# Optimization experiments

Measured on AMD Instinct MI355X. Metric: run time of the kernel, lower is better.

The kernel has to match this reference:

```python
import jax, jax.numpy as jnp
import numpy as np

N_NODES = 200000
N_EDGES = 6400000
N_GRAPHS = 512
VOCAB = 10
EMBED = 8
RLEN = 20
EPS = 1e-5


def setup_inputs() -> dict:
    key = jax.random.key(0)
    ks = jax.random.split(key, 16)
    f = lambda i, shape, s: jax.random.normal(ks[i], shape, jnp.float32) * s
    return {
        "x": jax.random.normal(ks[0], (N_NODES, 3), jnp.float32),
        "W1": f(1, (3, 64), 0.5), "b1": jnp.zeros((64,), jnp.float32),
        "gamma1": jnp.ones((64,), jnp.float32), "beta1": jnp.zeros((64,), jnp.float32),
        "W2": f(2, (64, 64), 0.12), "b2": jnp.zeros((64,), jnp.float32),
        "gamma2": jnp.ones((64,), jnp.float32), "beta2": jnp.zeros((64,), jnp.float32),
        "emb": f(3, (VOCAB, EMBED), 1.0),
        "conv_w": f(4, (16, EMBED, 3), 0.2), "conv_b": jnp.zeros((16,), jnp.float32),
        "fc_w": f(5, (16 * RLEN, 64), 0.06), "fc_b": jnp.zeros((64,), jnp.float32),
        "m1_w": f(6, (192, 128), 0.08), "m1_b": jnp.zeros((128,), jnp.float32),
        "m2_w": f(7, (128, 64), 0.1), "m2_b": jnp.zeros((64,), jnp.float32),
        "m3_w": f(8, (64, 3), 0.17), "m3_b": jnp.zeros((3,), jnp.float32),
        "edge_index": jax.random.randint(ks[9], (2, N_EDGES), 0, N_NODES),
        "batch": jnp.sort(jax.random.randint(ks[10], (N_NODES,), 0, N_GRAPHS)),
        "recipe": jax.random.randint(ks[11], (N_GRAPHS, RLEN), 0, VOCAB),
    }


def _gcn_aggregate(h, src, dst, dinv, n):
    # symmetric-normalized scatter-add: sum_j (d_i d_j)^{-1/2} h_j
    norm = dinv[src] * dinv[dst]
    return jax.ops.segment_sum(h[src] * norm[:, None], dst, num_segments=n)


def _bn(h, gamma, beta):
    mu = h.mean(0)
    var = h.var(0)  # biased variance, as torch BN uses for normalization
    return (h - mu) * jax.lax.rsqrt(var + EPS) * gamma + beta


def reference(x, W1, b1, gamma1, beta1, W2, b2, gamma2, beta2, emb,
              conv_w, conv_b, fc_w, fc_b, m1_w, m1_b, m2_w, m2_b, m3_w, m3_b,
              edge_index, batch, recipe):
    n = x.shape[0]
    loop = jnp.arange(n)
    src = jnp.concatenate([edge_index[0], loop])  # add self loops (GCNConv default)
    dst = jnp.concatenate([edge_index[1], loop])
    deg = jax.ops.segment_sum(jnp.ones_like(src, jnp.float32), dst, num_segments=n)
    dinv = jnp.where(deg > 0, jax.lax.rsqrt(deg), 0.0)

    h = _gcn_aggregate(x @ W1, src, dst, dinv, n) + b1
    h = jax.nn.relu(_bn(h, gamma1, beta1))
    h = _gcn_aggregate(h @ W2, src, dst, dinv, n) + b2
    h = jax.nn.relu(_bn(h, gamma2, beta2))

    counts = jax.ops.segment_sum(jnp.ones((n,), jnp.float32), batch, num_segments=N_GRAPHS)
    h_mean = jax.ops.segment_sum(h, batch, num_segments=N_GRAPHS) / jnp.maximum(counts, 1.0)[:, None]
    h_max = jax.ops.segment_max(h, batch, num_segments=N_GRAPHS)
    h_max = jnp.where(jnp.isfinite(h_max), h_max, 0.0)  # guard empty graphs
    h_graph = jnp.concatenate([h_mean, h_max], axis=1)  # [G, 128]

    r = emb[recipe].transpose(0, 2, 1)  # [G, embed, L]
    rc = jax.lax.conv_general_dilated(r, conv_w, window_strides=(1,), padding=[(1, 1)],
                                      dimension_numbers=("NCH", "OIH", "NCH"))
    rc = jax.nn.relu(rc + conv_b[None, :, None])  # [G, 16, L]
    r_flat = rc.reshape(rc.shape[0], -1)  # channel-major flatten, matches torch
    r_vec = jax.nn.relu(r_flat @ fc_w + fc_b)  # [G, 64]

    c = jnp.concatenate([h_graph, r_vec], axis=1)  # [G, 192]
    c = jax.nn.relu(c @ m1_w + m1_b)
    c = jax.nn.relu(c @ m2_w + m2_b)
    return c @ m3_w + m3_b  # [G, 3]
```

## Files before the change

kernel.cpp:

```cpp
#include <hip/hip_runtime.h>

#define N_NODES 200000
#define N_EDGES 6400000
#define N_GRAPHS 512
#define RLEN 20
#define EMBED 8
#define EPS 1e-5f

#define NPB 1024
#define NBKT ((N_NODES + NPB - 1) / NPB)
#define CHUNK 4096
#define CAP 36864

typedef unsigned short ushort_t;
typedef __attribute__((ext_vector_type(8))) short short8;
typedef __attribute__((ext_vector_type(4))) float f32x4;

__device__ inline ushort_t f32_to_bf16(float f) {
  unsigned u = __float_as_uint(f);
  unsigned r = (u + 0x7fff + ((u >> 16) & 1)) >> 16;
  return (ushort_t)r;
}
__device__ inline float bf16_to_f32(ushort_t us) {
  return __uint_as_float(((unsigned)us) << 16);
}
__device__ inline float bfu_lo(unsigned u) { return __uint_as_float(u << 16); }
__device__ inline float bfu_hi(unsigned u) { return __uint_as_float(u & 0xFFFF0000u); }


__global__ void k_binit(int* __restrict__ bcursor) {
  int b = threadIdx.x;
  if (b < NBKT) bcursor[b] = b * CAP;
}

__global__ void __launch_bounds__(256) k_bscatter(const int* __restrict__ src,
                                                  const int* __restrict__ dst,
                                                  int* __restrict__ bcursor,
                                                  int* __restrict__ ebuf) {
  __shared__ int hist[256];
  __shared__ int scanb[256];
  __shared__ int gbase[NBKT];
  __shared__ int staged[CHUNK];
  __shared__ int addrs[CHUNK];
  __shared__ int s_total;
  int t = threadIdx.x;
  int e0 = blockIdx.x * CHUNK;
  hist[t] = 0;
  __syncthreads();

  int pk[16], bk[16], rk[16];
  #pragma unroll
  for (int k = 0; k < 16; ++k) {
    int idx = e0 + t + k * 256;
    bk[k] = -1;
    if (idx < N_EDGES) {
      int s = src[idx], d = dst[idx];
      int b = d >> 10;
      pk[k] = s | ((d & (NPB - 1)) << 18);
      bk[k] = b;
      rk[k] = atomicAdd(&hist[b], 1);
    }
  }
  __syncthreads();
  int hv = hist[t];
  scanb[t] = hv;
  __syncthreads();
  for (int off = 1; off < 256; off <<= 1) {
    int u = (t >= off) ? scanb[t - off] : 0;
    __syncthreads();
    scanb[t] += u;
    __syncthreads();
  }
  int offt = scanb[t] - hv;
  if (t < NBKT && hv > 0) gbase[t] = atomicAdd(&bcursor[t], hv);
  if (t == 255) s_total = scanb[255];
  __syncthreads();
  hist[t] = offt;
  __syncthreads();
  #pragma unroll
  for (int k = 0; k < 16; ++k) {
    if (bk[k] >= 0) {
      int slot = hist[bk[k]] + rk[k];
      staged[slot] = pk[k];
      addrs[slot] = gbase[bk[k]] + rk[k];
    }
  }
  __syncthreads();
  int total = s_total;
  for (int i = t; i < total; i += 256)
    ebuf[addrs[i]] = staged[i];
}

__global__ void __launch_bounds__(256) k_bfill(const int* __restrict__ bcursor,
                                               const int* __restrict__ ebuf,
                                               const float* __restrict__ x,
                                               int* __restrict__ rowstart,
                                               int* __restrict__ rowlen,
                                               float* __restrict__ dinv,
                                               float4* __restrict__ xs,
                                               int* __restrict__ cols) {
  __shared__ int deg[NPB];
  __shared__ int cur[NPB];
  __shared__ int wsum[4];
  int b = blockIdx.x;
  int t = threadIdx.x;
  int lane = t & 63, wid = t >> 6;
  int estart = b * CAP;
  int eend = bcursor[b];
  for (int i = t; i < NPB; i += 256) deg[i] = 0;
  __syncthreads();
  for (int i = estart + t; i < eend; i += 256) {
    int p = ebuf[i];
    atomicAdd(&deg[((unsigned)p) >> 18], 1);
  }
  __syncthreads();
  int d0 = deg[t * 4], d1 = deg[t * 4 + 1], d2 = deg[t * 4 + 2], d3 = deg[t * 4 + 3];
  int tsum = d0 + d1 + d2 + d3;
  int incl = tsum;
  #pragma unroll
  for (int off = 1; off < 64; off <<= 1) {
    int u = __shfl_up(incl, off);
    if (lane >= off) incl += u;
  }
  if (lane == 63) wsum[wid] = incl;
  int wexcl = incl - tsum;
  __syncthreads();
  int wbase = 0;
  for (int w = 0; w < wid; ++w) wbase += wsum[w];
  int ebase = wbase + wexcl;
  cur[t * 4 + 0] = ebase;
  cur[t * 4 + 1] = ebase + d0;
  cur[t * 4 + 2] = ebase + d0 + d1;
  cur[t * 4 + 3] = ebase + d0 + d1 + d2;
  __syncthreads();
  #pragma unroll
  for (int k = 0; k < 4; ++k) {
    int dl = t * 4 + k;
    int n = b * NPB + dl;
    if (n < N_NODES) {
      rowstart[n] = estart + cur[dl];
      rowlen[n] = deg[dl];
      float dv = rsqrtf((float)(deg[dl] + 1));
      dinv[n] = dv;
      float4 v;
      v.x = x[n * 3 + 0] * dv;
      v.y = x[n * 3 + 1] * dv;
      v.z = x[n * 3 + 2] * dv;
      v.w = 0.f;
      xs[n] = v;
    }
  }
  __syncthreads();
  for (int i = estart + t; i < eend; i += 256) {
    int p = ebuf[i];
    int dl = ((unsigned)p) >> 18;
    int lpos = atomicAdd(&cur[dl], 1);
    cols[estart + lpos] = p & 0x3FFFF;
  }
}


__global__ void k_agg1(const float4* __restrict__ xs, float4* __restrict__ t,
                       const int* __restrict__ rowstart, const int* __restrict__ rowlen,
                       const int* __restrict__ cols,
                       const float* __restrict__ dinv, float* __restrict__ mom) {
  int n = blockIdx.x * blockDim.x + threadIdx.x;
  float m9[9] = {0.f, 0.f, 0.f, 0.f, 0.f, 0.f, 0.f, 0.f, 0.f};
  if (n < N_NODES) {
    float4 self = xs[n];
    float a0 = self.x, a1 = self.y, a2 = self.z;
    float b0 = 0.f, b1 = 0.f, b2 = 0.f;
    float c0 = 0.f, c1 = 0.f, c2 = 0.f;
    float e0 = 0.f, e1 = 0.f, e2 = 0.f;
    int base = rowstart[n];
    int len = rowlen[n];
    int j = 0;
    for (; j + 8 <= len; j += 8) {
      int s0 = cols[base + j],     s1 = cols[base + j + 1];
      int s2 = cols[base + j + 2], s3 = cols[base + j + 3];
      int s4 = cols[base + j + 4], s5 = cols[base + j + 5];
      int s6 = cols[base + j + 6], s7 = cols[base + j + 7];
      float4 v0 = xs[s0], v1 = xs[s1], v2 = xs[s2], v3 = xs[s3];
      float4 v4 = xs[s4], v5 = xs[s5], v6 = xs[s6], v7 = xs[s7];
      a0 += v0.x + v4.x; a1 += v0.y + v4.y; a2 += v0.z + v4.z;
      b0 += v1.x + v5.x; b1 += v1.y + v5.y; b2 += v1.z + v5.z;
      c0 += v2.x + v6.x; c1 += v2.y + v6.y; c2 += v2.z + v6.z;
      e0 += v3.x + v7.x; e1 += v3.y + v7.y; e2 += v3.z + v7.z;
    }
    for (; j + 4 <= len; j += 4) {
      int s0 = cols[base + j], s1 = cols[base + j + 1];
      int s2 = cols[base + j + 2], s3 = cols[base + j + 3];
      float4 v0 = xs[s0], v1 = xs[s1], v2 = xs[s2], v3 = xs[s3];
      a0 += v0.x; a1 += v0.y; a2 += v0.z;
      b0 += v1.x; b1 += v1.y; b2 += v1.z;
      c0 += v2.x; c1 += v2.y; c2 += v2.z;
      e0 += v3.x; e1 += v3.y; e2 += v3.z;
    }
    for (; j < len; ++j) {
      float4 v = xs[cols[base + j]];
      a0 += v.x; a1 += v.y; a2 += v.z;
    }
    float dv = dinv[n];
    float4 o;
    o.x = dv * ((a0 + b0) + (c0 + e0));
    o.y = dv * ((a1 + b1) + (c1 + e1));
    o.z = dv * ((a2 + b2) + (c2 + e2));
    o.w = 0.f;
    t[n] = o;
    m9[0] = o.x; m9[1] = o.y; m9[2] = o.z;
    m9[3] = o.x * o.x; m9[4] = o.x * o.y; m9[5] = o.x * o.z;
    m9[6] = o.y * o.y; m9[7] = o.y * o.z; m9[8] = o.z * o.z;
  }
  #pragma unroll
  for (int off = 32; off; off >>= 1) {
    #pragma unroll
    for (int i = 0; i < 9; ++i) m9[i] += __shfl_xor(m9[i], off);
  }
  __shared__ float ls[4][9];
  int lane = threadIdx.x & 63, wid = threadIdx.x >> 6;
  if (lane == 0) {
    #pragma unroll
    for (int i = 0; i < 9; ++i) ls[wid][i] = m9[i];
  }
  __syncthreads();
  if (threadIdx.x < 9) {
    float s = ls[0][threadIdx.x] + ls[1][threadIdx.x] + ls[2][threadIdx.x] + ls[3][threadIdx.x];
    atomicAdd(&mom[threadIdx.x], s);
  }
}

__global__ void __launch_bounds__(256) k_l2m2(const float4* __restrict__ t,
                                              ushort_t* __restrict__ hb,
                                              const float* __restrict__ W1,
                                              const float* __restrict__ W2,
                                              const float* __restrict__ mom,
                                              const float* __restrict__ gamma,
                                              const float* __restrict__ beta,
                                              const float* __restrict__ dinv) {
  __shared__ float w1s[192];
  __shared__ ushort_t w2t_hi[64 * 64];
  __shared__ ushort_t w2t_lo[64 * 64];
  __shared__ float tt[4][16][4];
  __shared__ ushort_t at_hi[4][16 * 64];
  __shared__ ushort_t at_lo[4][16 * 64];
  int tix = threadIdx.x;
  int lane = tix & 63, wid = tix >> 6;
  if (tix < 192) w1s[tix] = W1[tix];
  for (int i = tix; i < 64 * 64; i += 256) {
    int f = i >> 6, k = i & 63;
    float w = W2[k * 64 + f];
    ushort_t hi = f32_to_bf16(w);
    w2t_hi[i] = hi;
    w2t_lo[i] = f32_to_bf16(w - bf16_to_f32(hi));
  }
  __syncthreads();

  int col = lane & 15, kb = lane >> 4;
  short8 bhi[4][2], blo[4][2];
  #pragma unroll
  for (int nt = 0; nt < 4; ++nt) {
    #pragma unroll
    for (int ks = 0; ks < 2; ++ks) {
      int base = (nt * 16 + col) * 64 + ks * 32 + kb * 8;
      bhi[nt][ks] = *reinterpret_cast<const short8*>(&w2t_hi[base]);
      blo[nt][ks] = *reinterpret_cast<const short8*>(&w2t_lo[base]);
    }
  }

  float inv_n = 1.0f / N_NODES;
  float w0 = w1s[lane], w1 = w1s[64 + lane], w2 = w1s[128 + lane];
  float mu = (mom[0] * w0 + mom[1] * w1 + mom[2] * w2) * inv_n;
  float eh2 = (mom[3] * w0 * w0 + 2.f * mom[4] * w0 * w1 + 2.f * mom[5] * w0 * w2 +
               mom[6] * w1 * w1 + 2.f * mom[7] * w1 * w2 + mom[8] * w2 * w2) * inv_n;
  float var = eh2 - mu * mu;
  float sc = rsqrtf(var + EPS) * gamma[lane];
  float sh = beta[lane] - mu * sc;

  for (int bt = blockIdx.x; bt < 3125; bt += gridDim.x) {
    int n0 = (bt * 4 + wid) * 16;
    if (lane < 16) {
      float4 v = t[n0 + lane];
      tt[wid][lane][0] = v.x; tt[wid][lane][1] = v.y; tt[wid][lane][2] = v.z;
    }
    #pragma unroll 4
    for (int i = 0; i < 16; ++i) {
      float h = tt[wid][i][0] * w0 + tt[wid][i][1] * w1 + tt[wid][i][2] * w2;
      float a = h * sc + sh;
      a = a > 0.f ? a : 0.f;
      ushort_t hi = f32_to_bf16(a);
      at_hi[wid][i * 64 + lane] = hi;
      at_lo[wid][i * 64 + lane] = f32_to_bf16(a - bf16_to_f32(hi));
    }
    short8 ahi[2], alo[2];
    #pragma unroll
    for (int ks = 0; ks < 2; ++ks) {
      int base = col * 64 + ks * 32 + kb * 8;
      ahi[ks] = *reinterpret_cast<const short8*>(&at_hi[wid][base]);
      alo[ks] = *reinterpret_cast<const short8*>(&at_lo[wid][base]);
    }
    float dv[4];
    #pragma unroll
    for (int r = 0; r < 4; ++r) dv[r] = dinv[n0 + kb * 4 + r];

    #pragma unroll
    for (int nt = 0; nt < 4; ++nt) {
      f32x4 acc = {0.f, 0.f, 0.f, 0.f};
      #pragma unroll
      for (int ks = 0; ks < 2; ++ks) {
        acc = __builtin_amdgcn_mfma_f32_16x16x32_bf16(ahi[ks], bhi[nt][ks], acc, 0, 0, 0);
        acc = __builtin_amdgcn_mfma_f32_16x16x32_bf16(ahi[ks], blo[nt][ks], acc, 0, 0, 0);
        acc = __builtin_amdgcn_mfma_f32_16x16x32_bf16(alo[ks], bhi[nt][ks], acc, 0, 0, 0);
      }
      #pragma unroll
      for (int r = 0; r < 4; ++r) {
        int node = n0 + kb * 4 + r;
        int feat = nt * 16 + col;
        hb[node * 64 + feat] = f32_to_bf16(acc[r] * dv[r]);
      }
    }
  }
}

__global__ void k_agg2(const ushort_t* __restrict__ hb, ushort_t* __restrict__ h1b,
                       const int* __restrict__ rowstart, const int* __restrict__ rowlen,
                       const int* __restrict__ cols, const float* __restrict__ dinv) {
  int node = blockIdx.x * 4 + (threadIdx.x >> 6);
  int lane = threadIdx.x & 63;
  if (node >= N_NODES) return;
  int half = lane >> 5;
  int fl = lane & 31;
  const unsigned* hb32 = (const unsigned*)hb;
  unsigned* o32 = (unsigned*)h1b;
  float2 acc;
  if (half == 0) {
    unsigned u = hb32[node * 32 + fl];
    acc.x = bfu_lo(u); acc.y = bfu_hi(u);
  } else { acc.x = 0.f; acc.y = 0.f; }
  int base = rowstart[node];
  int len = rowlen[node];
  for (int c0 = 0; c0 < len; c0 += 64) {
    int rem = len - c0;
    int m = rem < 64 ? rem : 64;
    int cidx = (lane < m) ? cols[base + c0 + lane] : 0;
    int j = 0;
    for (; j + 8 <= m; j += 8) {
      int sA = __shfl(cidx, j + half);
      int sB = __shfl(cidx, j + 2 + half);
      int sC = __shfl(cidx, j + 4 + half);
      int sD = __shfl(cidx, j + 6 + half);
      unsigned uA = hb32[sA * 32 + fl], uB = hb32[sB * 32 + fl];
      unsigned uC = hb32[sC * 32 + fl], uD = hb32[sD * 32 + fl];
      acc.x += (bfu_lo(uA) + bfu_lo(uB)) + (bfu_lo(uC) + bfu_lo(uD));
      acc.y += (bfu_hi(uA) + bfu_hi(uB)) + (bfu_hi(uC) + bfu_hi(uD));
    }
    for (; j + 2 <= m; j += 2) {
      int s = __shfl(cidx, j + half);
      unsigned u = hb32[s * 32 + fl];
      acc.x += bfu_lo(u);
      acc.y += bfu_hi(u);
    }
    if (j < m) {
      int s = __shfl(cidx, j);
      if (half == 0) {
        unsigned u = hb32[s * 32 + fl];
        acc.x += bfu_lo(u);
        acc.y += bfu_hi(u);
      }
    }
  }
  acc.x += __shfl_xor(acc.x, 32);
  acc.y += __shfl_xor(acc.y, 32);
  if (half == 0) {
    float dv = dinv[node];
    float ox = acc.x * dv, oy = acc.y * dv;
    o32[node * 32 + fl] = ((unsigned)f32_to_bf16(oy) << 16) | (unsigned)f32_to_bf16(ox);
  }
}

__global__ void k_bnstats_b(const ushort_t* __restrict__ h1b, float* __restrict__ stats) {
  const unsigned* h32 = (const unsigned*)h1b;
  int tid = threadIdx.x;
  int lane = tid & 63, wid = tid >> 6;
  int fl = lane & 31, rsel = lane >> 5;
  float s0 = 0.f, s1 = 0.f, q0 = 0.f, q1 = 0.f;
  for (int r = blockIdx.x * 8 + wid * 2 + rsel; r < N_NODES; r += gridDim.x * 8) {
    unsigned u = h32[r * 32 + fl];
    float a = bfu_lo(u), b = bfu_hi(u);
    s0 += a; s1 += b; q0 += a * a; q1 += b * b;
  }
  s0 += __shfl_xor(s0, 32); s1 += __shfl_xor(s1, 32);
  q0 += __shfl_xor(q0, 32); q1 += __shfl_xor(q1, 32);
  __shared__ float ls[4][64], lq[4][64];
  if (rsel == 0) {
    ls[wid][2 * fl] = s0; ls[wid][2 * fl + 1] = s1;
    lq[wid][2 * fl] = q0; lq[wid][2 * fl + 1] = q1;
  }
  __syncthreads();
  if (tid < 64) {
    float a = ls[0][tid] + ls[1][tid] + ls[2][tid] + ls[3][tid];
    float b = lq[0][tid] + lq[1][tid] + lq[2][tid] + lq[3][tid];
    atomicAdd(&stats[tid], a);
    atomicAdd(&stats[64 + tid], b);
  }
}


__global__ void k_gstart(const int* __restrict__ batch, int* __restrict__ gstart) {
  int g = blockIdx.x * blockDim.x + threadIdx.x;
  if (g > N_GRAPHS) return;
  int lo = 0, hi = N_NODES;
  while (lo < hi) {
    int mid = (lo + hi) >> 1;
    if (batch[mid] < g) lo = mid + 1; else hi = mid;
  }
  gstart[g] = lo;
}

__global__ void k_pool(const ushort_t* __restrict__ h1b, const float* __restrict__ stats2,
                       const float* __restrict__ gamma, const float* __restrict__ beta,
                       const int* __restrict__ gstart, float* __restrict__ hgraph) {
  __shared__ float ssum[4][64], smax[4][64];
  int g = blockIdx.x;
  int lane = threadIdx.x & 63, wid = threadIdx.x >> 6;
  int s0 = gstart[g], s1 = gstart[g + 1];
  float mu = stats2[lane] * (1.0f / N_NODES);
  float var = stats2[64 + lane] * (1.0f / N_NODES) - mu * mu;
  float sc = rsqrtf(var + EPS) * gamma[lane];
  float sh = beta[lane] - mu * sc;
  float sum = 0.f, mx = 0.f;
  for (int r = s0 + wid; r < s1; r += 4) {
    float v = bf16_to_f32(h1b[r * 64 + lane]) * sc + sh;
    v = v > 0.f ? v : 0.f;
    sum += v;
    mx = v > mx ? v : mx;
  }
  ssum[wid][lane] = sum;
  smax[wid][lane] = mx;
  __syncthreads();
  if (wid == 0) {
    float s = ssum[0][lane] + ssum[1][lane] + ssum[2][lane] + ssum[3][lane];
    float m = fmaxf(fmaxf(smax[0][lane], smax[1][lane]), fmaxf(smax[2][lane], smax[3][lane]));
    int cnt = s1 - s0;
    float inv = 1.0f / (float)(cnt > 0 ? cnt : 1);
    hgraph[g * 128 + lane] = s * inv;
    hgraph[g * 128 + 64 + lane] = m;
  }
}

__global__ void k_head(const float* __restrict__ hgraph,
                       const float* __restrict__ emb, const int* __restrict__ recipe,
                       const float* __restrict__ conv_w, const float* __restrict__ conv_b,
                       const float* __restrict__ fc_w, const float* __restrict__ fc_b,
                       const float* __restrict__ m1_w, const float* __restrict__ m1_b,
                       const float* __restrict__ m2_w, const float* __restrict__ m2_b,
                       const float* __restrict__ m3_w, const float* __restrict__ m3_b,
                       float* __restrict__ out) {
  __shared__ float r_s[RLEN][EMBED];
  __shared__ float convout[16 * RLEN];
  __shared__ float cvec[192];
  __shared__ float y1[128];
  __shared__ float y2[64];
  __shared__ int rec_s[RLEN];
  __shared__ float emb_s[80];
  int g = blockIdx.x;
  int t = threadIdx.x;
  if (t < 80) emb_s[t] = emb[t];
  if (t < RLEN) rec_s[t] = recipe[g * RLEN + t];
  __syncthreads();
  for (int idx = t; idx < RLEN * EMBED; idx += blockDim.x) {
    int pos = idx >> 3, e = idx & 7;
    r_s[pos][e] = emb_s[rec_s[pos] * EMBED + e];
  }
  if (t < 128) cvec[t] = hgraph[g * 128 + t];
  __syncthreads();
  for (int idx = t; idx < 16 * RLEN; idx += blockDim.x) {
    int c = idx / RLEN, pos = idx % RLEN;
    float acc = conv_b[c];
    #pragma unroll
    for (int k = 0; k < 3; ++k) {
      int p = pos + k - 1;
      if (p >= 0 && p < RLEN) {
        #pragma unroll
        for (int e = 0; e < EMBED; ++e)
          acc = fmaf(r_s[p][e], conv_w[(c * EMBED + e) * 3 + k], acc);
      }
    }
    convout[c * RLEN + pos] = acc > 0.f ? acc : 0.f;
  }
  __syncthreads();
  if (t < 64) {
    float acc = fc_b[t];
    for (int i = 0; i < 320; ++i) acc = fmaf(convout[i], fc_w[i * 64 + t], acc);
    cvec[128 + t] = acc > 0.f ? acc : 0.f;
  }
  __syncthreads();
  if (t < 128) {
    float acc = m1_b[t];
    for (int i = 0; i < 192; ++i) acc = fmaf(cvec[i], m1_w[i * 128 + t], acc);
    y1[t] = acc > 0.f ? acc : 0.f;
  }
  __syncthreads();
  if (t < 64) {
    float acc = m2_b[t];
    for (int i = 0; i < 128; ++i) acc = fmaf(y1[i], m2_w[i * 64 + t], acc);
    y2[t] = acc > 0.f ? acc : 0.f;
  }
  __syncthreads();
  if (t < 3) {
    float acc = m3_b[t];
    for (int i = 0; i < 64; ++i) acc = fmaf(y2[i], m3_w[i * 3 + t], acc);
    out[g * 3 + t] = acc;
  }
}

extern "C" void kernel_launch(void* const* d_in, const int* in_sizes, int n_in,
                              void* d_out, int out_size, void* d_ws, size_t ws_size,
                              hipStream_t stream) {
  const float* x      = (const float*)d_in[0];
  const float* W1     = (const float*)d_in[1];
  const float* gamma1 = (const float*)d_in[3];
  const float* beta1  = (const float*)d_in[4];
  const float* W2     = (const float*)d_in[5];
  const float* gamma2 = (const float*)d_in[7];
  const float* beta2  = (const float*)d_in[8];
  const float* emb    = (const float*)d_in[9];
  const float* conv_w = (const float*)d_in[10];
  const float* conv_b = (const float*)d_in[11];
  const float* fc_w   = (const float*)d_in[12];
  const float* fc_b   = (const float*)d_in[13];
  const float* m1_w   = (const float*)d_in[14];
  const float* m1_b   = (const float*)d_in[15];
  const float* m2_w   = (const float*)d_in[16];
  const float* m2_b   = (const float*)d_in[17];
  const float* m3_w   = (const float*)d_in[18];
  const float* m3_b   = (const float*)d_in[19];
  const int* ei       = (const int*)d_in[20];
  const int* batch    = (const int*)d_in[21];
  const int* recipe   = (const int*)d_in[22];
  const int* e_src = ei;
  const int* e_dst = ei + N_EDGES;
  float* out = (float*)d_out;

  char* p = (char*)d_ws;
  auto alloc = [&](size_t bytes) {
    char* r = p;
    p += (bytes + 255) & ~(size_t)255;
    return (void*)r;
  };
  int*   bcursor  = (int*)alloc((size_t)NBKT * 4);
  float* dinv     = (float*)alloc((size_t)N_NODES * 4);
  int*   rowstart = (int*)alloc((size_t)N_NODES * 4);
  int*   rowlen   = (int*)alloc((size_t)N_NODES * 4);
  int*   gstart   = (int*)alloc((size_t)(N_GRAPHS + 1) * 4);
  float* stats    = (float*)alloc(256 * 4);
  float* mom      = (float*)alloc(16 * 4);
  float* hgraph   = (float*)alloc((size_t)N_GRAPHS * 128 * 4);
  int*   cols     = (int*)alloc((size_t)NBKT * CAP * 4);
  float4* xs      = (float4*)alloc((size_t)N_NODES * 16);
  float4* tbuf    = (float4*)alloc((size_t)N_NODES * 16);
  int*   ebuf     = (int*)alloc((size_t)NBKT * CAP * 4);
  ushort_t* hb    = (ushort_t*)alloc((size_t)N_NODES * 64 * 2);
  ushort_t* h1b   = (ushort_t*)ebuf;

  hipMemsetAsync(stats, 0, 256 * 4, stream);
  hipMemsetAsync(mom, 0, 16 * 4, stream);

  k_binit<<<1, 256, 0, stream>>>(bcursor);
  k_bscatter<<<(N_EDGES + CHUNK - 1) / CHUNK, 256, 0, stream>>>(e_src, e_dst, bcursor, ebuf);
  k_bfill<<<NBKT, 256, 0, stream>>>(bcursor, ebuf, x, rowstart, rowlen, dinv, xs, cols);
  k_agg1<<<(N_NODES + 255) / 256, 256, 0, stream>>>(xs, tbuf, rowstart, rowlen, cols, dinv, mom);
  k_l2m2<<<625, 256, 0, stream>>>(tbuf, hb, W1, W2, mom, gamma1, beta1, dinv);
  k_agg2<<<(N_NODES + 3) / 4, 256, 0, stream>>>(hb, h1b, rowstart, rowlen, cols, dinv);
  k_bnstats_b<<<512, 256, 0, stream>>>(h1b, stats);
  k_gstart<<<1, 576, 0, stream>>>(batch, gstart);
  k_pool<<<N_GRAPHS, 256, 0, stream>>>(h1b, stats, gamma2, beta2, gstart, hgraph);
  k_head<<<N_GRAPHS, 128, 0, stream>>>(hgraph, emb, recipe, conv_w, conv_b, fc_w, fc_b,
                                       m1_w, m1_b, m2_w, m2_b, m3_w, m3_b, out);
}
```

Before: 439.1 us.

## Vectorize edge loads and scatter bucket writes directly without LDS staging

The bucket-scatter kernel now reads src/dst as int4 vectors and drops the block-wide prefix scan and LDS staging. Each edge is written straight to its global bucket slot using its per-bucket atomic rank. The bucket-fill kernel also reads packed edges as int4 in both its degree and column passes. This trades coalesced staged writes for fewer barriers and less LDS use, at the risk of more scattered global stores.

```diff
diff --git a/kernel.cpp b/kernel.cpp
--- a/kernel.cpp
+++ b/kernel.cpp
@@ -38,57 +38,44 @@
                                                   int* __restrict__ bcursor,
                                                   int* __restrict__ ebuf) {
   __shared__ int hist[256];
-  __shared__ int scanb[256];
-  __shared__ int gbase[NBKT];
-  __shared__ int staged[CHUNK];
-  __shared__ int addrs[CHUNK];
-  __shared__ int s_total;
+  __shared__ int gbase[256];
   int t = threadIdx.x;
+  hist[t] = 0;
+  __syncthreads();
+
+  const int4* src4 = (const int4*)(src + blockIdx.x * CHUNK);
+  const int4* dst4 = (const int4*)(dst + blockIdx.x * CHUNK);
   int e0 = blockIdx.x * CHUNK;
-  hist[t] = 0;
-  __syncthreads();
+  int nrem = N_EDGES - e0;
+  int nv = (nrem >= CHUNK ? CHUNK : nrem) >> 2;
 
   int pk[16], bk[16], rk[16];
   #pragma unroll
-  for (int k = 0; k < 16; ++k) {
-    int idx = e0 + t + k * 256;
-    bk[k] = -1;
-    if (idx < N_EDGES) {
-      int s = src[idx], d = dst[idx];
-      int b = d >> 10;
-      pk[k] = s | ((d & (NPB - 1)) << 18);
-      bk[k] = b;
-      rk[k] = atomicAdd(&hist[b], 1);
-    }
-  }
-  __syncthreads();
-  int hv = hist[t];
-  scanb[t] = hv;
-  __syncthreads();
-  for (int off = 1; off < 256; off <<= 1) {
-    int u = (t >= off) ? scanb[t - off] : 0;
-    __syncthreads();
-    scanb[t] += u;
-    __syncthreads();
-  }
-  int offt = scanb[t] - hv;
-  if (t < NBKT && hv > 0) gbase[t] = atomicAdd(&bcursor[t], hv);
-  if (t == 255) s_total = scanb[255];
-  __syncthreads();
-  hist[t] = offt;
+  for (int g = 0; g < 4; ++g) {
+    int vi = g * 256 + t;
+    if (vi < nv) {
+      int4 s4 = src4[vi];
+      int4 d4 = dst4[vi];
+      #pragma unroll
+      for (int c = 0; c < 4; ++c) {
+        int s = (&s4.x)[c], d = (&d4.x)[c];
+        int b = d >> 10;
+        pk[g * 4 + c] = s | ((d & (NPB - 1)) << 18);
+        bk[g * 4 + c] = b;
+        rk[g * 4 + c] = atomicAdd(&hist[b], 1);
+      }
+    } else {
+      #pragma unroll
+      for (int c = 0; c < 4; ++c) bk[g * 4 + c] = -1;
+    }
+  }
+  __syncthreads();
+  if (t < NBKT && hist[t] > 0) gbase[t] = atomicAdd(&bcursor[t], hist[t]);
   __syncthreads();
   #pragma unroll
   for (int k = 0; k < 16; ++k) {
-    if (bk[k] >= 0) {
-      int slot = hist[bk[k]] + rk[k];
-      staged[slot] = pk[k];
-      addrs[slot] = gbase[bk[k]] + rk[k];
-    }
-  }
-  __syncthreads();
-  int total = s_total;
-  for (int i = t; i < total; i += 256)
-    ebuf[addrs[i]] = staged[i];
+    if (bk[k] >= 0) ebuf[gbase[bk[k]] + rk[k]] = pk[k];
+  }
 }
 
 __global__ void __launch_bounds__(256) k_bfill(const int* __restrict__ bcursor,
@@ -107,9 +94,19 @@
   int lane = t & 63, wid = t >> 6;
   int estart = b * CAP;
   int eend = bcursor[b];
+  int cnt = eend - estart;
+  int nv = cnt >> 2;
+  const int4* eb4 = (const int4*)(ebuf + estart);
   for (int i = t; i < NPB; i += 256) deg[i] = 0;
   __syncthreads();
-  for (int i = estart + t; i < eend; i += 256) {
+  for (int i = t; i < nv; i += 256) {
+    int4 p4 = eb4[i];
+    atomicAdd(&deg[((unsigned)p4.x) >> 18], 1);
+    atomicAdd(&deg[((unsigned)p4.y) >> 18], 1);
+    atomicAdd(&deg[((unsigned)p4.z) >> 18], 1);
+    atomicAdd(&deg[((unsigned)p4.w) >> 18], 1);
+  }
+  for (int i = estart + (nv << 2) + t; i < eend; i += 256) {
     int p = ebuf[i];
     atomicAdd(&deg[((unsigned)p) >> 18], 1);
   }
@@ -151,7 +148,17 @@
     }
   }
   __syncthreads();
-  for (int i = estart + t; i < eend; i += 256) {
+  for (int i = t; i < nv; i += 256) {
+    int4 p4 = eb4[i];
+    #pragma unroll
+    for (int c = 0; c < 4; ++c) {
+      int p = (&p4.x)[c];
+      int dl = ((unsigned)p) >> 18;
+      int lpos = atomicAdd(&cur[dl], 1);
+      cols[estart + lpos] = p & 0x3FFFF;
+    }
+  }
+  for (int i = estart + (nv << 2) + t; i < eend; i += 256) {
     int p = ebuf[i];
     int dl = ((unsigned)p) >> 18;
     int lpos = atomicAdd(&cur[dl], 1);
```

Result: faster. 428.1 us (-2.5%).
